# Optimization experiments

Measured on AMD Instinct MI355X. Metric: run time of the kernel, lower is better.

The kernel has to match this reference:

```python
import jax, jax.numpy as jnp
import numpy as np

B, L1, L2, D = 128, 256, 256, 768
NEG = -10000.0
EPS = 1e-8


def setup_inputs() -> dict:
    key = jax.random.key(0)
    k1, k2, k3, k4 = jax.random.split(key, 4)
    v1 = jax.random.normal(k1, (B, L1, D), dtype=jnp.float32)
    v2 = jax.random.normal(k2, (B, L2, D), dtype=jnp.float32)
    # masks from random valid lengths in [L//2, L]
    len1 = jax.random.randint(k3, (B,), L1 // 2, L1 + 1)
    len2 = jax.random.randint(k4, (B,), L2 // 2, L2 + 1)
    mask1 = (jnp.arange(L1)[None, :] < len1[:, None]).astype(jnp.float32)
    mask2 = (jnp.arange(L2)[None, :] < len2[:, None]).astype(jnp.float32)
    return {"v1": v1, "mask1": mask1, "v2": v2, "mask2": mask2}


def reference(v1, mask1, v2, mask2):
    # alignment matrix [B, L1, L2]
    match = jnp.einsum('bld,bmd->blm', v1, v2)
    pair_mask = (mask1[:, :, None] * mask2[:, None, :]) > 0
    match = jnp.where(pair_mask, match, NEG)
    # attention over side 1: negative max-pool over L2, scaled
    s1 = -jnp.max(match, axis=2) / 100.0            # [B, L1]
    s1 = jnp.where(mask1 > 0, s1, NEG)
    attn1 = jax.nn.softmax(s1, axis=1)
    p1 = jnp.einsum('bld,bl->bd', v1, attn1)        # [B, D]
    # attention over side 2: negative max-pool over L1, scaled
    s2 = -jnp.max(match, axis=1) / 100.0            # [B, L2]
    s2 = jnp.where(mask2 > 0, s2, NEG)
    attn2 = jax.nn.softmax(s2, axis=1)
    p2 = jnp.einsum('bmd,bm->bd', v2, attn2)        # [B, D]
    # torch.nn.functional.cosine_similarity semantics (per-vector norm clamp)
    n1 = jnp.maximum(jnp.linalg.norm(p1, axis=-1), EPS)
    n2 = jnp.maximum(jnp.linalg.norm(p2, axis=-1), EPS)
    return jnp.sum(p1 * p2, axis=-1) / (n1 * n2)
```

## Files before the change

### kernel.cpp

```cpp
#include <hip/hip_runtime.h>


#define B_   128
#define L_   256
#define D_   768
#define NEGV (-10000.0f)

typedef _Float16 f16x8 __attribute__((ext_vector_type(8)));
typedef float    f32x4 __attribute__((ext_vector_type(4)));

#define BT   128
#define BKH  64
#define NKT  (D_ / BKH)

__device__ __forceinline__ unsigned fmap(float f) {
    unsigned u = __float_as_uint(f);
    return (u & 0x80000000u) ? ~u : (u | 0x80000000u);
}
__device__ __forceinline__ float fdecode(unsigned u) {
    return __uint_as_float((u & 0x80000000u) ? (u ^ 0x80000000u) : ~u);
}
__device__ __forceinline__ float wred_max(float v) {
    #pragma unroll
    for (int o = 32; o; o >>= 1) v = fmaxf(v, __shfl_xor(v, o));
    return v;
}
__device__ __forceinline__ float wred_sum(float v) {
    #pragma unroll
    for (int o = 32; o; o >>= 1) v += __shfl_xor(v, o);
    return v;
}

__global__ __launch_bounds__(512, 4)
void k_match_max(const float* __restrict__ v1, const float* __restrict__ m1,
                 const float* __restrict__ v2, const float* __restrict__ m2,
                 unsigned* __restrict__ ru1, unsigned* __restrict__ ru2)
{
    __shared__ __align__(16) _Float16 As[BT * BKH];
    __shared__ __align__(16) _Float16 Bs[BT * BKH];
    __shared__ unsigned rU[BT], cU[BT];
    __shared__ float m1s[BT], m2s[BT];

    const int bid = blockIdx.x;
    const int wg  = (bid & 7) * 64 + (bid >> 3);
    const int b = wg >> 2, ti = (wg >> 1) & 1, tj = wg & 1;

    const int t = threadIdx.x;
    const int lane = t & 63, w = t >> 6;
    const int wr = w >> 1, wc = w & 1;
    const int fr = lane & 15, fg = lane >> 4;

    if (t < BT) {
        rU[t] = 0u; cU[t] = 0u;
        m1s[t] = m1[b * L_ + ti * BT + t];
        m2s[t] = m2[b * L_ + tj * BT + t];
    }

    const float* pa = v1 + ((size_t)b * L_ + ti * BT) * D_;
    const float* pb = v2 + ((size_t)b * L_ + tj * BT) * D_;

    float4 ra[2][2], rb[2][2];

    #define LOADT(kt)                                                          \
        _Pragma("unroll")                                                      \
        for (int g = 0; g < 2; ++g) {                                          \
            int idx = g * 512 + t;                   \
            int row = idx >> 3;                                                \
            int cf  = (kt) * BKH + ((idx & 7) << 3);                           \
            const float* A  = pa + (size_t)row * D_ + cf;                      \
            const float* Bp = pb + (size_t)row * D_ + cf;                      \
            ra[g][0] = *(const float4*)A;  ra[g][1] = *(const float4*)(A + 4); \
            rb[g][0] = *(const float4*)Bp; rb[g][1] = *(const float4*)(Bp + 4);\
        }

    f32x4 acc[2][4] = {};
    LOADT(0);
    for (int kt = 0; kt < NKT; ++kt) {
        __syncthreads();
        #pragma unroll
        for (int g = 0; g < 2; ++g) {
            int idx = g * 512 + t;
            int row = idx >> 3;
            int blk = (idx & 7) ^ (row & 7);
            f16x8 ah, bh;
            #pragma unroll
            for (int q = 0; q < 4; ++q) {
                ah[q] = (_Float16)ra[g][0][q]; ah[4 + q] = (_Float16)ra[g][1][q];
                bh[q] = (_Float16)rb[g][0][q]; bh[4 + q] = (_Float16)rb[g][1][q];
            }
            *(f16x8*)&As[row * BKH + blk * 8] = ah;
            *(f16x8*)&Bs[row * BKH + blk * 8] = bh;
        }
        __syncthreads();
        if (kt + 1 < NKT) { LOADT(kt + 1); }
        __builtin_amdgcn_sched_barrier(0);
        #pragma unroll
        for (int ks = 0; ks < 2; ++ks) {
            f16x8 af[2], bf[4];
            #pragma unroll
            for (int i = 0; i < 2; ++i) {
                int r1 = wr * 32 + i * 16 + fr;
                af[i] = *(const f16x8*)&As[r1 * BKH + (((ks * 4 + fg) ^ (r1 & 7)) << 3)];
            }
            #pragma unroll
            for (int j = 0; j < 4; ++j) {
                int r2 = wc * 64 + j * 16 + fr;
                bf[j] = *(const f16x8*)&Bs[r2 * BKH + (((ks * 4 + fg) ^ (r2 & 7)) << 3)];
            }
            #pragma unroll
            for (int i = 0; i < 2; ++i)
                #pragma unroll
                for (int j = 0; j < 4; ++j)
                    acc[i][j] = __builtin_amdgcn_mfma_f32_16x16x32_f16(af[i], bf[j], acc[i][j], 0, 0, 0);
        }
    }
    #undef LOADT

    #pragma unroll
    for (int i = 0; i < 2; ++i)
        #pragma unroll
        for (int r = 0; r < 4; ++r) {
            int row = wr * 32 + i * 16 + fg * 4 + r;
            bool rv = m1s[row] > 0.f;
            float mx = NEGV;
            #pragma unroll
            for (int j = 0; j < 4; ++j) {
                int col = wc * 64 + j * 16 + fr;
                float vv = (rv && m2s[col] > 0.f) ? acc[i][j][r] : NEGV;
                mx = fmaxf(mx, vv);
            }
            atomicMax(&rU[row], fmap(mx));
        }
    #pragma unroll
    for (int j = 0; j < 4; ++j) {
        int col = wc * 64 + j * 16 + fr;
        bool cv = m2s[col] > 0.f;
        float mx = NEGV;
        #pragma unroll
        for (int i = 0; i < 2; ++i)
            #pragma unroll
            for (int r = 0; r < 4; ++r) {
                int row = wr * 32 + i * 16 + fg * 4 + r;
                float vv = (cv && m1s[row] > 0.f) ? acc[i][j][r] : NEGV;
                mx = fmaxf(mx, vv);
            }
        atomicMax(&cU[col], fmap(mx));
    }
    __syncthreads();
    if (t < BT)            atomicMax(&ru1[b * L_ + ti * BT + t], rU[t]);
    else if (t < 2 * BT)   atomicMax(&ru2[b * L_ + tj * BT + (t - BT)], cU[t - BT]);
}

__global__ __launch_bounds__(256)
void k_attn_pool(const float* __restrict__ v1, const float* __restrict__ m1,
                 const float* __restrict__ v2, const float* __restrict__ m2,
                 const unsigned* __restrict__ ru1, const unsigned* __restrict__ ru2,
                 float* __restrict__ pout)
{
    const int lin = (int)blockIdx.x;
    const int swz = (lin & 7) * 96 + (lin >> 3);
    const int b = swz / 6, rem = swz % 6, side = rem / 3, chunk = rem % 3;

    const float* v     = side ? v2 : v1;
    const float* mk    = side ? m2 : m1;
    const unsigned* ru = side ? ru2 : ru1;
    const int t = threadIdx.x, lane = t & 63, w = t >> 6;

    __shared__ float attn[L_];
    __shared__ float sred[4];

    float mkv = mk[b * L_ + t];
    float s = (mkv > 0.f) ? (-fdecode(ru[b * L_ + t]) / 100.0f) : NEGV;

    float wm = wred_max(s);
    if (lane == 0) sred[w] = wm;
    __syncthreads();
    float mx = fmaxf(fmaxf(sred[0], sred[1]), fmaxf(sred[2], sred[3]));
    float e = expf(s - mx);
    __syncthreads();
    float ws = wred_sum(e);
    if (lane == 0) sred[w] = ws;
    __syncthreads();
    float sum = sred[0] + sred[1] + sred[2] + sred[3];
    attn[t] = e / sum;
    __syncthreads();

    const int d = chunk * 256 + t;
    const float* vb = v + (size_t)b * L_ * D_ + d;
    float p = 0.f;
    #pragma unroll 8
    for (int l = 0; l < L_; ++l) p += attn[l] * vb[(size_t)l * D_];
    pout[((size_t)b * 2 + side) * D_ + d] = p;
}

__global__ __launch_bounds__(256)
void k_cos(const float* __restrict__ pout, float* __restrict__ out)
{
    const int b = blockIdx.x, t = threadIdx.x, lane = t & 63, w = t >> 6;
    const float* p1 = pout + (size_t)b * 2 * D_;
    const float* p2 = p1 + D_;
    float dot = 0.f, n1 = 0.f, n2 = 0.f;
    for (int d = t; d < D_; d += 256) {
        float a = p1[d], c = p2[d];
        dot += a * c; n1 += a * a; n2 += c * c;
    }
    dot = wred_sum(dot); n1 = wred_sum(n1); n2 = wred_sum(n2);
    __shared__ float sd[4], sa[4], sc[4];
    if (lane == 0) { sd[w] = dot; sa[w] = n1; sc[w] = n2; }
    __syncthreads();
    if (t == 0) {
        float dd = sd[0] + sd[1] + sd[2] + sd[3];
        float aa = sa[0] + sa[1] + sa[2] + sa[3];
        float cc = sc[0] + sc[1] + sc[2] + sc[3];
        out[b] = dd / (fmaxf(sqrtf(aa), 1e-8f) * fmaxf(sqrtf(cc), 1e-8f));
    }
}

extern "C" void kernel_launch(void* const* d_in, const int* in_sizes, int n_in,
                              void* d_out, int out_size, void* d_ws, size_t ws_size,
                              hipStream_t stream)
{
    const float* v1 = (const float*)d_in[0];
    const float* m1 = (const float*)d_in[1];
    const float* v2 = (const float*)d_in[2];
    const float* m2 = (const float*)d_in[3];
    float* out = (float*)d_out;

    unsigned* ru1 = (unsigned*)d_ws;
    unsigned* ru2 = ru1 + (size_t)B_ * L_;
    float*    pout = (float*)(ru2 + (size_t)B_ * L_);

    hipMemsetAsync(d_ws, 0, 2 * (size_t)B_ * L_ * sizeof(unsigned), stream);

    k_match_max<<<dim3((L_ / BT) * (L_ / BT) * B_), 512, 0, stream>>>(v1, m1, v2, m2, ru1, ru2);

    k_attn_pool<<<dim3(B_ * 2 * 3), 256, 0, stream>>>(v1, m1, v2, m2, ru1, ru2, pout);

    k_cos<<<B_, 256, 0, stream>>>(pout, out);
}
```

Baseline: 80.28 us.

## Stream fp32 tiles directly to LDS with double buffering, convert on read

```diff
diff --git a/kernel.cpp b/kernel.cpp
--- a/kernel.cpp
+++ b/kernel.cpp
@@ -7,11 +7,12 @@
 #define NEGV (-10000.0f)
 
 typedef _Float16 f16x8 __attribute__((ext_vector_type(8)));
+typedef __fp16   h16x2 __attribute__((ext_vector_type(2)));
 typedef float    f32x4 __attribute__((ext_vector_type(4)));
 
 #define BT   128
-#define BKH  64
-#define NKT  (D_ / BKH)
+#define BK   32
+#define NKT  (D_ / BK)
 
 __device__ __forceinline__ unsigned fmap(float f) {
     unsigned u = __float_as_uint(f);
@@ -29,6 +30,21 @@
     #pragma unroll
     for (int o = 32; o; o >>= 1) v += __shfl_xor(v, o);
     return v;
+}
+
+__device__ __forceinline__ void gll16(const float* g, void* lds) {
+    __builtin_amdgcn_global_load_lds(
+        (const __attribute__((address_space(1))) void*)g,
+        (__attribute__((address_space(3))) void*)lds, 16, 0, 0);
+}
+
+__device__ __forceinline__ f16x8 cvt8(float4 a, float4 b) {
+    union { h16x2 h2[4]; f16x8 h8; } u;
+    u.h2[0] = __builtin_amdgcn_cvt_pkrtz(a.x, a.y);
+    u.h2[1] = __builtin_amdgcn_cvt_pkrtz(a.z, a.w);
+    u.h2[2] = __builtin_amdgcn_cvt_pkrtz(b.x, b.y);
+    u.h2[3] = __builtin_amdgcn_cvt_pkrtz(b.z, b.w);
+    return u.h8;
 }
 
 __global__ __launch_bounds__(512, 4)
@@ -36,8 +52,8 @@
                  const float* __restrict__ v2, const float* __restrict__ m2,
                  unsigned* __restrict__ ru1, unsigned* __restrict__ ru2)
 {
-    __shared__ __align__(16) _Float16 As[BT * BKH];
-    __shared__ __align__(16) _Float16 Bs[BT * BKH];
+    __shared__ __align__(16) float As[2][BT * BK];
+    __shared__ __align__(16) float Bs[2][BT * BK];
     __shared__ unsigned rU[BT], cU[BT];
     __shared__ float m1s[BT], m2s[BT];
 
@@ -59,62 +75,55 @@
     const float* pa = v1 + ((size_t)b * L_ + ti * BT) * D_;
     const float* pb = v2 + ((size_t)b * L_ + tj * BT) * D_;
 
-    float4 ra[2][2], rb[2][2];
-
-    #define LOADT(kt)                                                          \
-        _Pragma("unroll")                                                      \
-        for (int g = 0; g < 2; ++g) {                                          \
-            int idx = g * 512 + t;                   \
-            int row = idx >> 3;                                                \
-            int cf  = (kt) * BKH + ((idx & 7) << 3);                           \
-            const float* A  = pa + (size_t)row * D_ + cf;                      \
-            const float* Bp = pb + (size_t)row * D_ + cf;                      \
-            ra[g][0] = *(const float4*)A;  ra[g][1] = *(const float4*)(A + 4); \
-            rb[g][0] = *(const float4*)Bp; rb[g][1] = *(const float4*)(Bp + 4);\
+    const int r_in = lane >> 3;
+    const int sblk = (lane & 7) ^ r_in;
+    const int row0 = (w * 2 + 0) * 8 + r_in;
+    const int row1 = (w * 2 + 1) * 8 + r_in;
+    const float* ga0 = pa + (size_t)row0 * D_ + sblk * 4;
+    const float* ga1 = pa + (size_t)row1 * D_ + sblk * 4;
+    const float* gb0 = pb + (size_t)row0 * D_ + sblk * 4;
+    const float* gb1 = pb + (size_t)row1 * D_ + sblk * 4;
+
+    #define STAGE(buf, kt) do {                                   \
+        int ko = (kt) * BK;                                       \
+        gll16(ga0 + ko, &As[buf][(w * 2 + 0) * 256]);             \
+        gll16(ga1 + ko, &As[buf][(w * 2 + 1) * 256]);             \
+        gll16(gb0 + ko, &Bs[buf][(w * 2 + 0) * 256]);             \
+        gll16(gb1 + ko, &Bs[buf][(w * 2 + 1) * 256]);             \
+    } while (0)
+
+    f32x4 acc[2][4] = {};
+    STAGE(0, 0);
+    __syncthreads();
+    int cur = 0;
+    for (int kt = 0; kt < NKT; ++kt) {
+        if (kt + 1 < NKT) STAGE(cur ^ 1, kt + 1);
+        f16x8 af[2], bf[4];
+        #pragma unroll
+        for (int i = 0; i < 2; ++i) {
+            int r1 = wr * 32 + i * 16 + fr;
+            const float* base = &As[cur][r1 * BK];
+            float4 x = *(const float4*)(base + (((2 * fg + 0) ^ (fr & 7)) << 2));
+            float4 y = *(const float4*)(base + (((2 * fg + 1) ^ (fr & 7)) << 2));
+            af[i] = cvt8(x, y);
         }
-
-    f32x4 acc[2][4] = {};
-    LOADT(0);
-    for (int kt = 0; kt < NKT; ++kt) {
+        #pragma unroll
+        for (int j = 0; j < 4; ++j) {
+            int r2 = wc * 64 + j * 16 + fr;
+            const float* base = &Bs[cur][r2 * BK];
+            float4 x = *(const float4*)(base + (((2 * fg + 0) ^ (fr & 7)) << 2));
+            float4 y = *(const float4*)(base + (((2 * fg + 1) ^ (fr & 7)) << 2));
+            bf[j] = cvt8(x, y);
+        }
+        #pragma unroll
+        for (int i = 0; i < 2; ++i)
+            #pragma unroll
+            for (int j = 0; j < 4; ++j)
+                acc[i][j] = __builtin_amdgcn_mfma_f32_16x16x32_f16(af[i], bf[j], acc[i][j], 0, 0, 0);
         __syncthreads();
-        #pragma unroll
-        for (int g = 0; g < 2; ++g) {
-            int idx = g * 512 + t;
-            int row = idx >> 3;
-            int blk = (idx & 7) ^ (row & 7);
-            f16x8 ah, bh;
-            #pragma unroll
-            for (int q = 0; q < 4; ++q) {
-                ah[q] = (_Float16)ra[g][0][q]; ah[4 + q] = (_Float16)ra[g][1][q];
-                bh[q] = (_Float16)rb[g][0][q]; bh[4 + q] = (_Float16)rb[g][1][q];
-            }
-            *(f16x8*)&As[row * BKH + blk * 8] = ah;
-            *(f16x8*)&Bs[row * BKH + blk * 8] = bh;
-        }
-        __syncthreads();
-        if (kt + 1 < NKT) { LOADT(kt + 1); }
-        __builtin_amdgcn_sched_barrier(0);
-        #pragma unroll
-        for (int ks = 0; ks < 2; ++ks) {
-            f16x8 af[2], bf[4];
-            #pragma unroll
-            for (int i = 0; i < 2; ++i) {
-                int r1 = wr * 32 + i * 16 + fr;
-                af[i] = *(const f16x8*)&As[r1 * BKH + (((ks * 4 + fg) ^ (r1 & 7)) << 3)];
-            }
-            #pragma unroll
-            for (int j = 0; j < 4; ++j) {
-                int r2 = wc * 64 + j * 16 + fr;
-                bf[j] = *(const f16x8*)&Bs[r2 * BKH + (((ks * 4 + fg) ^ (r2 & 7)) << 3)];
-            }
-            #pragma unroll
-            for (int i = 0; i < 2; ++i)
-                #pragma unroll
-                for (int j = 0; j < 4; ++j)
-                    acc[i][j] = __builtin_amdgcn_mfma_f32_16x16x32_f16(af[i], bf[j], acc[i][j], 0, 0, 0);
-        }
-    }
-    #undef LOADT
+        cur ^= 1;
+    }
+    #undef STAGE
 
     #pragma unroll
     for (int i = 0; i < 2; ++i)
@@ -230,7 +239,7 @@
     unsigned* ru2 = ru1 + (size_t)B_ * L_;
     float*    pout = (float*)(ru2 + (size_t)B_ * L_);
 
-    hipMemsetAsync(d_ws, 0, 2 * (size_t)B_ * L_ * sizeof(unsigned), stream);
+    (void)hipMemsetAsync(d_ws, 0, 2 * (size_t)B_ * L_ * sizeof(unsigned), stream);
 
     k_match_max<<<dim3((L_ / BT) * (L_ / BT) * B_), 512, 0, stream>>>(v1, m1, v2, m2, ru1, ru2);
 
```

After: 77.33 us. 1.04x faster.
